# Kernel optimization log

Hardware: AMD Instinct MI355X
Metric: run time of the kernel (lower is better)

Reference implementation:

```python
import jax, jax.numpy as jnp
import numpy as np

N, IN_DIM, OUT_DIM, NUM_HOPS, SD = 8192, 256, 256, 4, 64
ETA, LAM_LAP, LAM_SP, EPS = 0.5, 0.3, 0.05, 0.5
LN_EPS = 1e-5


def setup_inputs() -> dict:
    key = jax.random.key(0)
    ks = jax.random.split(key, 6)
    K = NUM_HOPS + 1
    return {
        "H": jax.random.normal(ks[0], (N, IN_DIM), jnp.float32),
        "hops": jax.random.normal(ks[1], (K, N, IN_DIM), jnp.float32),
        "L": jax.random.normal(ks[2], (N, N), jnp.float32),
        "U": jax.random.normal(ks[3], (K, IN_DIM, SD), jnp.float32) * 0.1,
        "W_in": jax.random.normal(ks[4], (OUT_DIM, IN_DIM), jnp.float32) * 0.05,
        "ln_gamma": jnp.ones((OUT_DIM,), jnp.float32),
        "ln_beta": jnp.zeros((OUT_DIM,), jnp.float32),
        "log_tau": jnp.zeros((), jnp.float32),
    }


def _per_hop(U_k, H_k):
    n = H_k.shape[0]
    Q, _ = jnp.linalg.qr(U_k)                 # [in_dim, sd]
    Z = Q.T @ H_k.T                           # [sd, n]
    G = Z @ Z.T                               # [sd, sd] Gram, reused
    Sigma = G / (n + 1e-8)
    tr_S = jnp.trace(Sigma)
    tr_S2 = jnp.sum(Sigma * Sigma)            # trace(Sigma @ Sigma), Sigma symmetric
    rank_eff = tr_S ** 2 / (tr_S2 + 1e-8)
    coeff = SD / (n * EPS ** 2 + 1e-8)
    M = jnp.eye(SD, dtype=Z.dtype) + coeff * G
    Lc = jnp.linalg.cholesky(M)
    MiZ = jax.scipy.linalg.cho_solve((Lc, True), Z)  # [sd, n]
    grad_R = (Q @ MiZ).T                      # [n, in_dim]
    return rank_eff, grad_R


def reference(H, hops, L, U, W_in, ln_gamma, ln_beta, log_tau):
    tau = jnp.clip(jnp.exp(log_tau), 0.1, 10.0)
    rank_effs, grads_R = jax.vmap(_per_hop)(U, hops)      # [K], [K,n,in_dim]
    lap_terms = jnp.einsum('nm,kmd->knd', L, hops)        # [K,n,in_dim]
    w = jax.nn.softmax(rank_effs / tau)                   # [K]
    grad_sum = jnp.einsum('k,knd->nd', w, grads_R)
    lap_sum = jnp.einsum('k,knd->nd', w, lap_terms)
    H_half = H + ETA * grad_sum - ETA * LAM_LAP * lap_sum
    H_prox = jnp.sign(H_half) * jax.nn.relu(jnp.abs(H_half) - LAM_SP * ETA)
    H_out = H_prox @ W_in.T
    mu = jnp.mean(H_out, axis=-1, keepdims=True)
    var = jnp.var(H_out, axis=-1, keepdims=True)
    H_out = (H_out - mu) * jax.lax.rsqrt(var + LN_EPS) * ln_gamma + ln_beta
    return H_out, rank_effs, w
```

## Files before the change

kernel.cpp:

```cpp
#include <hip/hip_runtime.h>
#include <stdint.h>


typedef __attribute__((ext_vector_type(8))) short  s16x8;
typedef __attribute__((ext_vector_type(4))) float  f32x4;

#define NNODE 8192
#define DIN   256
#define KHOP  5
#define SDM   64

static const size_t OFF_Q    = 0;
static const size_t OFF_QT   = OFF_Q   + (size_t)5*256*64*4;
static const size_t OFF_ZT   = OFF_QT  + (size_t)5*64*256*2;
static const size_t OFF_GP   = OFF_ZT  + (size_t)5*8192*64*2;
static const size_t OFF_LM   = OFF_GP  + (size_t)5*16*4096*4;
static const size_t OFF_RD   = OFF_LM  + (size_t)5*4096*4;
static const size_t OFF_LU   = OFF_RD  + (size_t)5*64*4;
static const size_t OFF_RDU  = OFF_LU  + (size_t)5*4096*4;
static const size_t OFF_RE   = OFF_RDU + (size_t)5*64*4;
static const size_t OFF_W    = OFF_RE  + 64;
static const size_t OFF_T2   = OFF_W   + 64;
static const size_t OFF_HWT  = OFF_T2  + (size_t)5*256*64*2;
static const size_t OFF_WBF  = OFF_HWT + (size_t)256*8192*2;
static const size_t OFF_HP   = OFF_WBF + (size_t)256*256*2;
static const size_t OFF_PART = OFF_HP  + (size_t)8192*256*2;

__device__ __forceinline__ unsigned short f2bf(float f){
  unsigned u = __builtin_bit_cast(unsigned, f);
  u += 0x7FFFu + ((u >> 16) & 1u);
  return (unsigned short)(u >> 16);
}
__device__ __forceinline__ float bf2f(unsigned h){
  return __builtin_bit_cast(float, h << 16);
}
__device__ __forceinline__ void gl_lds16(const void* g, void* l){
  __builtin_amdgcn_global_load_lds(
      (const __attribute__((address_space(1))) void*)g,
      (__attribute__((address_space(3))) void*)l, 16, 0, 0);
}
__device__ __forceinline__ f32x4 mfma16(s16x8 a, s16x8 b, f32x4 c){
  return __builtin_amdgcn_mfma_f32_16x16x32_bf16(a, b, c, 0, 0, 0);
}
__device__ __forceinline__ int swz(int row7, int colbyte){
  return row7*128 + (colbyte ^ (row7 << 4));
}

__device__ __forceinline__ void wave_chol64(float* a, float& rdk, int lane){
  rdk = 0.0f;
  #pragma unroll
  for (int j = 0; j < 64; ++j){
    float dj  = __shfl(a[j], j);
    float d   = sqrtf(fmaxf(dj, 1e-20f));
    float rdj = 1.0f / d;
    float cj  = a[j] * rdj;
    a[j] = cj;
    if (lane == j) rdk = rdj;
    #pragma unroll
    for (int l = j+1; l < 64; ++l)
      a[l] -= cj * __shfl(cj, l);
  }
}

__global__ __launch_bounds__(256) void k_pre(const float* __restrict__ U,
                                             float* __restrict__ Lu,
                                             float* __restrict__ rdu){
  __shared__ float A[64*65];
  int tid = threadIdx.x;
  int k = blockIdx.x;
  const float* Uk = U + (size_t)k*16384;
  int ti = tid >> 4, tj = tid & 15;
  float s[16];
  #pragma unroll
  for (int i = 0; i < 16; ++i) s[i] = 0.0f;
  for (int n = 0; n < 256; ++n){
    f32x4 xa = *(const f32x4*)(Uk + n*64 + ti*4);
    f32x4 xb = *(const f32x4*)(Uk + n*64 + tj*4);
    #pragma unroll
    for (int p = 0; p < 4; ++p)
      #pragma unroll
      for (int q = 0; q < 4; ++q) s[p*4+q] += xa[p]*xb[q];
  }
  #pragma unroll
  for (int p = 0; p < 4; ++p)
    #pragma unroll
    for (int q = 0; q < 4; ++q) A[(ti*4+p)*65 + tj*4+q] = s[p*4+q];
  __syncthreads();
  if (tid < 64){
    int lane = tid;
    float a[64];
    #pragma unroll
    for (int l = 0; l < 64; ++l) a[l] = A[lane*65 + l];
    float rdk;
    wave_chol64(a, rdk, lane);
    #pragma unroll
    for (int l = 0; l < 64; ++l) Lu[(size_t)k*4096 + lane*64 + l] = a[l];
    rdu[k*64 + lane] = rdk;
  }
}

__global__ __launch_bounds__(256) void k_qsolve(const float* __restrict__ U,
                                                const float* __restrict__ Lu,
                                                const float* __restrict__ rdu,
                                                float* __restrict__ Qf,
                                                unsigned short* __restrict__ Qt){
  int k = blockIdx.y, tid = threadIdx.x, wave = tid >> 6, lane = tid & 63;
  __shared__ float Al[64*65];
  __shared__ float rds[64];
  for (int e = tid; e < 4096; e += 256) Al[(e>>6)*65 + (e&63)] = Lu[(size_t)k*4096 + e];
  if (tid < 64) rds[tid] = rdu[k*64 + tid];
  __syncthreads();
  int n = blockIdx.x*4 + wave;
  float x = U[((size_t)k*256 + n)*64 + lane];
  #pragma unroll
  for (int j = 0; j < 64; ++j){
    float zj = __shfl(x, j) * rds[j];
    x = (lane == j) ? zj : (lane > j ? x - Al[lane*65+j]*zj : x);
  }
  Qf[((size_t)k*256 + n)*64 + lane] = x;
  Qt[(size_t)k*16384 + lane*256 + n] = f2bf(x);
}

__global__ __launch_bounds__(256,2) void k_zgemm(const float* __restrict__ hops,
                                                 const unsigned short* __restrict__ Qt,
                                                 unsigned short* __restrict__ Zt){
  __shared__ __align__(16) unsigned short Al[128][72];
  __shared__ __align__(16) unsigned short Bl[64][64];
  int tid = threadIdx.x, lane = tid & 63, wave = tid >> 6;
  int q = lane >> 4, r = lane & 15;
  int k = blockIdx.y, m0 = blockIdx.x * 128;
  f32x4 acc[2][4];
  #pragma unroll
  for (int a = 0; a < 2; ++a)
    #pragma unroll
    for (int b = 0; b < 4; ++b) acc[a][b] = (f32x4){0,0,0,0};
  int rr = tid >> 1, half = tid & 1;
  for (int it = 0; it < 4; ++it){
    __syncthreads();
    #pragma unroll
    for (int i = 0; i < 2; ++i){
      int o = i*4096 + wave*1024 + lane*16;
      int srow = o >> 7, kc = (o & 127) >> 1;
      gl_lds16(Qt + (size_t)k*16384 + srow*256 + it*64 + kc,
               (char*)&Bl[0][0] + i*4096 + wave*1024);
    }
    const float* ga = hops + ((size_t)k*NNODE + m0 + rr)*256 + it*64 + half*32;
    f32x4 v[8];
    #pragma unroll
    for (int i = 0; i < 8; ++i) v[i] = *(const f32x4*)(ga + i*4);
    #pragma unroll
    for (int i = 0; i < 4; ++i){
      s16x8 t;
      #pragma unroll
      for (int j = 0; j < 8; ++j){ int e = i*8+j; t[j] = (short)f2bf(v[e>>2][e&3]); }
      *(s16x8*)&Al[rr][half*32 + i*8] = t;
    }
    __syncthreads();
    #pragma unroll
    for (int h = 0; h < 2; ++h){
      int ko = h*32 + q*8;
      s16x8 b[4];
      #pragma unroll
      for (int ni = 0; ni < 4; ++ni) b[ni] = *(const s16x8*)&Bl[ni*16 + r][ko];
      #pragma unroll
      for (int mi = 0; mi < 2; ++mi){
        s16x8 a = *(const s16x8*)&Al[wave*32 + mi*16 + r][ko];
        #pragma unroll
        for (int ni = 0; ni < 4; ++ni) acc[mi][ni] = mfma16(a, b[ni], acc[mi][ni]);
      }
    }
  }
  #pragma unroll
  for (int mi = 0; mi < 2; ++mi)
    #pragma unroll
    for (int ni = 0; ni < 4; ++ni)
      #pragma unroll
      for (int ii = 0; ii < 4; ++ii){
        int m = m0 + wave*32 + mi*16 + q*4 + ii;
        int sc = ni*16 + r;
        Zt[((size_t)k*NNODE + m)*64 + sc] = f2bf(acc[mi][ni][ii]);
      }
}

__global__ __launch_bounds__(256) void k_gpart(const unsigned short* __restrict__ Zt,
                                               float* __restrict__ Gp){
  int k = blockIdx.x, c = blockIdx.y, tid = threadIdx.x;
  __shared__ __align__(16) unsigned short Zl[128][64];
  int ti = tid >> 4, tj = tid & 15;
  float acc[16];
  #pragma unroll
  for (int i = 0; i < 16; ++i) acc[i] = 0.0f;
  for (int sub = 0; sub < 4; ++sub){
    const char* gb = (const char*)Zt + ((size_t)k*NNODE + c*512 + sub*128)*128;
    __syncthreads();
    #pragma unroll
    for (int i = 0; i < 4; ++i){
      int o = i*4096 + tid*16;
      *(uint4*)((char*)&Zl[0][0] + o) = *(const uint4*)(gb + o);
    }
    __syncthreads();
    for (int n = 0; n < 128; ++n){
      const unsigned short* row = &Zl[n][0];
      uint2 ua = *(const uint2*)(row + ti*4);
      uint2 ub = *(const uint2*)(row + tj*4);
      float xa[4] = { bf2f(ua.x & 0xffff), bf2f(ua.x >> 16), bf2f(ua.y & 0xffff), bf2f(ua.y >> 16) };
      float xb[4] = { bf2f(ub.x & 0xffff), bf2f(ub.x >> 16), bf2f(ub.y & 0xffff), bf2f(ub.y >> 16) };
      #pragma unroll
      for (int p = 0; p < 4; ++p)
        #pragma unroll
        for (int qn = 0; qn < 4; ++qn) acc[p*4+qn] += xa[p]*xb[qn];
    }
  }
  float* o = Gp + ((size_t)k*16 + c)*4096;
  #pragma unroll
  for (int p = 0; p < 4; ++p)
    #pragma unroll
    for (int qn = 0; qn < 4; ++qn) o[(ti*4+p)*64 + tj*4+qn] = acc[p*4+qn];
}

__global__ __launch_bounds__(256) void k_gred(const float* __restrict__ Gp,
                                              float* __restrict__ LmO,
                                              float* __restrict__ rdO,
                                              float* __restrict__ reO){
  int k = blockIdx.x, tid = threadIdx.x;
  __shared__ float A[64*65];
  __shared__ float red[256];
  int ti = tid >> 4, tj = tid & 15;
  float s[16];
  #pragma unroll
  for (int i = 0; i < 16; ++i) s[i] = 0.0f;
  for (int c = 0; c < 16; ++c){
    const float* g = Gp + ((size_t)k*16 + c)*4096 + (ti*4)*64 + tj*4;
    #pragma unroll
    for (int p = 0; p < 4; ++p)
      #pragma unroll
      for (int qn = 0; qn < 4; ++qn) s[p*4+qn] += g[p*64+qn];
  }
  const float sc    = 1.0f / (8192.0f + 1e-8f);
  const float coeff = 64.0f / (8192.0f*0.25f + 1e-8f);
  float trp = 0.0f, tr2p = 0.0f;
  #pragma unroll
  for (int p = 0; p < 4; ++p)
    #pragma unroll
    for (int qn = 0; qn < 4; ++qn){
      float gg = s[p*4+qn];
      float sg = gg * sc;
      tr2p += sg*sg;
      int row = ti*4+p, col = tj*4+qn;
      if (row == col) trp += sg;
      A[row*65 + col] = (row == col ? 1.0f : 0.0f) + coeff*gg;
    }
  red[tid] = trp; __syncthreads();
  for (int o = 128; o > 0; o >>= 1){ if (tid < o) red[tid] += red[tid+o]; __syncthreads(); }
  float tr = red[0]; __syncthreads();
  red[tid] = tr2p; __syncthreads();
  for (int o = 128; o > 0; o >>= 1){ if (tid < o) red[tid] += red[tid+o]; __syncthreads(); }
  float tr2 = red[0];
  if (tid == 0) reO[k] = tr*tr / (tr2 + 1e-8f);
  __syncthreads();
  if (tid < 64){
    int lane = tid;
    float a[64];
    #pragma unroll
    for (int l = 0; l < 64; ++l) a[l] = A[lane*65 + l];
    float rdk;
    wave_chol64(a, rdk, lane);
    #pragma unroll
    for (int l = 0; l < 64; ++l) LmO[(size_t)k*4096 + lane*64 + l] = a[l];
    rdO[k*64 + lane] = rdk;
  }
}

__global__ void k_soft(const float* __restrict__ re, const float* __restrict__ ltau,
                       float* __restrict__ wv, float* __restrict__ dtail){
  if (threadIdx.x == 0){
    float tau = expf(ltau[0]);
    tau = fminf(fmaxf(tau, 0.1f), 10.0f);
    float r[5], m = -1e30f;
    for (int i = 0; i < 5; ++i){ r[i] = re[i]; m = fmaxf(m, r[i]); }
    float e[5], sum = 0.0f;
    for (int i = 0; i < 5; ++i){ e[i] = expf((r[i]-m)/tau); sum += e[i]; }
    for (int i = 0; i < 5; ++i){
      float w = e[i]/sum;
      wv[i] = w; dtail[i] = r[i]; dtail[5+i] = w;
    }
  }
}

__global__ __launch_bounds__(256) void k_post(const float* __restrict__ hops,
                                              const float* __restrict__ wv,
                                              unsigned short* __restrict__ hwT,
                                              const float* __restrict__ Qf,
                                              const float* __restrict__ LmI,
                                              const float* __restrict__ rdI,
                                              unsigned short* __restrict__ T2w,
                                              const float* __restrict__ Win,
                                              unsigned short* __restrict__ Wbf){
  __shared__ float T[64*65];
  __shared__ float rds[64];
  int bid = blockIdx.x, tid = threadIdx.x;
  if (bid < 512){
    int n0 = (bid & 127)*64, d0 = (bid >> 7)*64;
    float wl[5];
    #pragma unroll
    for (int k = 0; k < 5; ++k) wl[k] = -0.15f * wv[k];
    for (int e = tid; e < 1024; e += 256){
      int row = e >> 4, c4 = (e & 15)*4;
      f32x4 acc = (f32x4){0,0,0,0};
      #pragma unroll
      for (int k = 0; k < 5; ++k){
        f32x4 v = *(const f32x4*)(hops + ((size_t)k*NNODE + n0 + row)*256 + d0 + c4);
        acc += v * wl[k];
      }
      T[row*65 + c4+0] = acc[0]; T[row*65 + c4+1] = acc[1];
      T[row*65 + c4+2] = acc[2]; T[row*65 + c4+3] = acc[3];
    }
    __syncthreads();
    for (int e = tid; e < 1024; e += 256){
      int dr = e >> 4, c4 = (e & 15)*4;
      unsigned short h0 = f2bf(T[(c4+0)*65 + dr]);
      unsigned short h1 = f2bf(T[(c4+1)*65 + dr]);
      unsigned short h2 = f2bf(T[(c4+2)*65 + dr]);
      unsigned short h3 = f2bf(T[(c4+3)*65 + dr]);
      uint2 u; u.x = (unsigned)h0 | ((unsigned)h1 << 16); u.y = (unsigned)h2 | ((unsigned)h3 << 16);
      *(uint2*)(hwT + (size_t)(d0+dr)*NNODE + n0 + c4) = u;
    }
  } else if (bid < 832){
    int i = bid - 512;
    int k = i >> 6, xb = i & 63;
    int wave = tid >> 6, lane = tid & 63;
    for (int e = tid; e < 4096; e += 256) T[(e>>6)*65 + (e&63)] = LmI[(size_t)k*4096 + e];
    if (tid < 64) rds[tid] = rdI[k*64 + tid];
    __syncthreads();
    int n = xb*4 + wave;
    float x = Qf[((size_t)k*256 + n)*64 + lane];
    #pragma unroll
    for (int j = 0; j < 64; ++j){
      float zj = __shfl(x, j) * rds[j];
      x = (lane == j) ? zj : (lane > j ? x - T[lane*65+j]*zj : x);
    }
    #pragma unroll
    for (int j = 63; j >= 0; --j){
      float yj = __shfl(x, j) * rds[j];
      x = (lane == j) ? yj : (lane < j ? x - T[j*65+lane]*yj : x);
    }
    float scale = 0.5f * wv[k];
    T2w[((size_t)k*256 + n)*64 + lane] = f2bf(scale * x);
  } else {
    int i = bid - 832;
    int e = (i*256 + tid)*4;
    f32x4 v = *(const f32x4*)(Win + e);
    uint2 u;
    u.x = (unsigned)f2bf(v[0]) | ((unsigned)f2bf(v[1]) << 16);
    u.y = (unsigned)f2bf(v[2]) | ((unsigned)f2bf(v[3]) << 16);
    *(uint2*)(Wbf + e) = u;
  }
}

__global__ __launch_bounds__(256,2) void k_grad(const unsigned short* __restrict__ Zt,
                                                const unsigned short* __restrict__ T2w,
                                                unsigned short* __restrict__ out8){
  __shared__ __align__(16) unsigned short SM[18432];
  char* Al = (char*)SM;
  char* Bl = (char*)SM + 4096;
  int tid = threadIdx.x, lane = tid & 63, wave = tid >> 6;
  int q = lane >> 4, r = lane & 15;
  int m0 = blockIdx.x * 32;
  int gr8 = lane >> 3;
  int gcS = ((lane & 7) ^ gr8) * 16;
  f32x4 acc[2][4];
  #pragma unroll
  for (int a = 0; a < 2; ++a)
    #pragma unroll
    for (int b = 0; b < 4; ++b) acc[a][b] = (f32x4){0,0,0,0};
  for (int kk = 0; kk < 5; ++kk){
    __syncthreads();
    {
      int grow = wave*8 + gr8;
      gl_lds16((const char*)Zt + ((size_t)kk*NNODE + m0 + grow)*128 + gcS,
               Al + wave*1024);
    }
    #pragma unroll
    for (int i = 0; i < 8; ++i){
      int cb = i*4 + wave;
      int grow = cb*8 + gr8;
      gl_lds16((const char*)T2w + (size_t)kk*32768 + (size_t)grow*128 + gcS,
               Bl + cb*1024);
    }
    __syncthreads();
    #pragma unroll
    for (int h = 0; h < 2; ++h){
      int kb = h*64 + q*16;
      s16x8 b[4];
      #pragma unroll
      for (int ni = 0; ni < 4; ++ni){
        int row = wave*64 + ni*16 + r;
        b[ni] = *(const s16x8*)(Bl + (row>>3)*1024 + swz(row&7, kb));
      }
      #pragma unroll
      for (int mi = 0; mi < 2; ++mi){
        int row = mi*16 + r;
        s16x8 a = *(const s16x8*)(Al + (row>>3)*1024 + swz(row&7, kb));
        #pragma unroll
        for (int ni = 0; ni < 4; ++ni) acc[mi][ni] = mfma16(a, b[ni], acc[mi][ni]);
      }
    }
  }
  #pragma unroll
  for (int mi = 0; mi < 2; ++mi)
    #pragma unroll
    for (int ni = 0; ni < 4; ++ni)
      #pragma unroll
      for (int ii = 0; ii < 4; ++ii){
        int m = m0 + mi*16 + q*4 + ii;
        int n = wave*64 + ni*16 + r;
        out8[(size_t)m*256 + n] = f2bf(acc[mi][ni][ii]);
      }
}

__global__ __launch_bounds__(512,1) void k_big(const float* __restrict__ Lf,
                                               const unsigned short* __restrict__ Bt,
                                               unsigned short* __restrict__ part){
  __shared__ __align__(16) unsigned short SM[24960];
  char* Al = (char*)SM;
  char* Bl = (char*)SM + 16*1040;
  int tid = threadIdx.x, lane = tid & 63, wave = tid >> 6;
  int q = lane >> 4, r = lane & 15;
  int wr = wave >> 2, wc = wave & 3;
  int m0 = (blockIdx.x & 63) * 128;
  int by = blockIdx.x >> 6;
  size_t kbase = (size_t)by * 1024;
  int sr = lane >> 3;
  int sc8b = ((lane & 7) ^ sr) * 8;
  int sc8a = (lane & 7) * 8;
  int adst = swz(sr, (lane & 7) * 16);
  f32x4 acc[4][4];
  #pragma unroll
  for (int a = 0; a < 4; ++a)
    #pragma unroll
    for (int b = 0; b < 4; ++b) acc[a][b] = (f32x4){0,0,0,0};
  {
    f32x4 av[2][2];
    #pragma unroll
    for (int i = 0; i < 2; ++i){
      int c = wave*2 + i;
      const float* p = Lf + (size_t)(m0 + c*8 + sr)*NNODE + kbase + sc8a;
      av[i][0] = *(const f32x4*)p;
      av[i][1] = *(const f32x4*)(p + 4);
    }
    #pragma unroll
    for (int i = 0; i < 4; ++i){
      int cb = wave*4 + i;
      gl_lds16(Bt + (size_t)(cb*8 + sr)*NNODE + kbase + sc8b,
               Bl + cb*1040);
    }
    #pragma unroll
    for (int i = 0; i < 2; ++i){
      int c = wave*2 + i;
      s16x8 t;
      #pragma unroll
      for (int e = 0; e < 8; ++e) t[e] = (short)f2bf(av[i][e>>2][e&3]);
      *(s16x8*)(Al + c*1040 + adst) = t;
    }
    __syncthreads();
  }
  for (int t = 0; t < 16; ++t){
    size_t kn = kbase + (size_t)(t+1)*64;
    f32x4 av[2][2];
    if (t < 15){
      #pragma unroll
      for (int i = 0; i < 2; ++i){
        int c = wave*2 + i;
        const float* p = Lf + (size_t)(m0 + c*8 + sr)*NNODE + kn + sc8a;
        av[i][0] = *(const f32x4*)p;
        av[i][1] = *(const f32x4*)(p + 4);
      }
    }
    #pragma unroll
    for (int h = 0; h < 2; ++h){
      int kb = h*64 + q*16;
      s16x8 b[4];
      #pragma unroll
      for (int ni = 0; ni < 4; ++ni){
        int d = wc*64 + ni*16 + r;
        b[ni] = *(const s16x8*)(Bl + (d>>3)*1040 + swz(d&7, kb));
      }
      #pragma unroll
      for (int mi = 0; mi < 4; ++mi){
        int m = wr*64 + mi*16 + r;
        s16x8 a = *(const s16x8*)(Al + (m>>3)*1040 + swz(m&7, kb));
        #pragma unroll
        for (int ni = 0; ni < 4; ++ni) acc[mi][ni] = mfma16(a, b[ni], acc[mi][ni]);
      }
    }
    __syncthreads();
    if (t < 15){
      #pragma unroll
      for (int i = 0; i < 4; ++i){
        int cb = wave*4 + i;
        gl_lds16(Bt + (size_t)(cb*8 + sr)*NNODE + kn + sc8b,
                 Bl + cb*1040);
      }
      #pragma unroll
      for (int i = 0; i < 2; ++i){
        int c = wave*2 + i;
        s16x8 tt;
        #pragma unroll
        for (int e = 0; e < 8; ++e) tt[e] = (short)f2bf(av[i][e>>2][e&3]);
        *(s16x8*)(Al + c*1040 + adst) = tt;
      }
    }
    __syncthreads();
  }
  unsigned short* o = part + (size_t)by * 2097152;
  #pragma unroll
  for (int mi = 0; mi < 4; ++mi)
    #pragma unroll
    for (int ni = 0; ni < 4; ++ni)
      #pragma unroll
      for (int ii = 0; ii < 4; ++ii){
        int m = m0 + wr*64 + mi*16 + q*4 + ii;
        int n = wc*64 + ni*16 + r;
        o[(size_t)m*256 + n] = f2bf(acc[mi][ni][ii]);
      }
}

__global__ __launch_bounds__(256,2) void k_finln(const float* __restrict__ H,
                                                 const unsigned short* __restrict__ part,
                                                 const unsigned short* __restrict__ Wbf,
                                                 const float* __restrict__ gamma,
                                                 const float* __restrict__ beta,
                                                 float* __restrict__ out){
  __shared__ __align__(16) unsigned short Hl[64][264];
  __shared__ __align__(16) unsigned short Bl[256][64];
  __shared__ float SmR[64][4];
  __shared__ float SqR[64][4];
  int tid = threadIdx.x, lane = tid & 63, wave = tid >> 6;
  int q = lane >> 4, r = lane & 15;
  int m0 = blockIdx.x * 64;
  #define PROX(a) ({ float _t = fabsf(a) - 0.025f; _t > 0.0f ? copysignf(_t,(a)) : 0.0f; })
  for (int g = tid; g < 4096; g += 256){
    int row = g >> 6, c4 = (g & 63) * 4;
    size_t e = (size_t)(m0 + row)*256 + c4;
    f32x4 h = *(const f32x4*)(H + e);
    float s0 = h[0], s1 = h[1], s2 = h[2], s3 = h[3];
    #pragma unroll
    for (int sl = 0; sl < 9; ++sl){
      uint2 u = *(const uint2*)(part + (size_t)sl*2097152 + e);
      s0 += bf2f(u.x & 0xffff); s1 += bf2f(u.x >> 16);
      s2 += bf2f(u.y & 0xffff); s3 += bf2f(u.y >> 16);
    }
    uint2 o;
    o.x = (unsigned)f2bf(PROX(s0)) | ((unsigned)f2bf(PROX(s1)) << 16);
    o.y = (unsigned)f2bf(PROX(s2)) | ((unsigned)f2bf(PROX(s3)) << 16);
    *(uint2*)&Hl[row][c4] = o;
  }
  f32x4 acc[4][4];
  #pragma unroll
  for (int a = 0; a < 4; ++a)
    #pragma unroll
    for (int b = 0; b < 4; ++b) acc[a][b] = (f32x4){0,0,0,0};
  for (int it = 0; it < 4; ++it){
    __syncthreads();
    #pragma unroll
    for (int i = 0; i < 8; ++i){
      int o = i*4096 + wave*1024 + lane*16;
      int n = o >> 7, kc = o & 127;
      gl_lds16((const char*)Wbf + (size_t)n*512 + it*128 + kc,
               (char*)&Bl[0][0] + i*4096 + wave*1024);
    }
    __syncthreads();
    #pragma unroll
    for (int h = 0; h < 2; ++h){
      int ko = it*64 + h*32 + q*8;
      s16x8 b[4];
      #pragma unroll
      for (int ni = 0; ni < 4; ++ni) b[ni] = *(const s16x8*)&Bl[wave*64 + ni*16 + r][h*32 + q*8];
      #pragma unroll
      for (int mi = 0; mi < 4; ++mi){
        s16x8 a = *(const s16x8*)&Hl[mi*16 + r][ko];
        #pragma unroll
        for (int ni = 0; ni < 4; ++ni) acc[mi][ni] = mfma16(a, b[ni], acc[mi][ni]);
      }
    }
  }
  #pragma unroll
  for (int mi = 0; mi < 4; ++mi)
    #pragma unroll
    for (int ii = 0; ii < 4; ++ii){
      float sm = 0.0f, sq = 0.0f;
      #pragma unroll
      for (int ni = 0; ni < 4; ++ni){
        float v = acc[mi][ni][ii];
        sm += v; sq += v*v;
      }
      #pragma unroll
      for (int o = 1; o < 16; o <<= 1){ sm += __shfl_xor(sm, o, 64); sq += __shfl_xor(sq, o, 64); }
      if (r == 0){
        int rl = mi*16 + q*4 + ii;
        SmR[rl][wave] = sm; SqR[rl][wave] = sq;
      }
    }
  __syncthreads();
  float g[4], b[4];
  #pragma unroll
  for (int ni = 0; ni < 4; ++ni){
    g[ni] = gamma[wave*64 + ni*16 + r];
    b[ni] = beta [wave*64 + ni*16 + r];
  }
  #pragma unroll
  for (int mi = 0; mi < 4; ++mi)
    #pragma unroll
    for (int ii = 0; ii < 4; ++ii){
      int rl = mi*16 + q*4 + ii;
      float sm = SmR[rl][0] + SmR[rl][1] + SmR[rl][2] + SmR[rl][3];
      float sq = SqR[rl][0] + SqR[rl][1] + SqR[rl][2] + SqR[rl][3];
      float mean = sm * (1.0f/256.0f);
      float var  = sq * (1.0f/256.0f) - mean*mean;
      float rs   = rsqrtf(var + 1e-5f);
      #pragma unroll
      for (int ni = 0; ni < 4; ++ni){
        out[(size_t)(m0+rl)*256 + wave*64 + ni*16 + r] =
            (acc[mi][ni][ii] - mean)*rs*g[ni] + b[ni];
      }
    }
}

extern "C" void kernel_launch(void* const* d_in, const int* in_sizes, int n_in,
                              void* d_out, int out_size, void* d_ws, size_t ws_size,
                              hipStream_t stream){
  const float* H    = (const float*)d_in[0];
  const float* hops = (const float*)d_in[1];
  const float* Lmat = (const float*)d_in[2];
  const float* U    = (const float*)d_in[3];
  const float* Win  = (const float*)d_in[4];
  const float* gam  = (const float*)d_in[5];
  const float* bet  = (const float*)d_in[6];
  const float* ltau = (const float*)d_in[7];
  float* out = (float*)d_out;

  char* ws = (char*)d_ws;
  float*          Qf   = (float*)(ws + OFF_Q);
  unsigned short* Qt   = (unsigned short*)(ws + OFF_QT);
  unsigned short* Zt   = (unsigned short*)(ws + OFF_ZT);
  float*          Gp   = (float*)(ws + OFF_GP);
  float*          Lm   = (float*)(ws + OFF_LM);
  float*          rdw  = (float*)(ws + OFF_RD);
  float*          Lu   = (float*)(ws + OFF_LU);
  float*          rdu  = (float*)(ws + OFF_RDU);
  float*          re   = (float*)(ws + OFF_RE);
  float*          wv   = (float*)(ws + OFF_W);
  unsigned short* T2w  = (unsigned short*)(ws + OFF_T2);
  unsigned short* hwT  = (unsigned short*)(ws + OFF_HWT);
  unsigned short* Wbf  = (unsigned short*)(ws + OFF_WBF);
  unsigned short* part = (unsigned short*)(ws + OFF_PART);

  hipLaunchKernelGGL(k_pre,    dim3(5),      dim3(256), 0, stream, U, Lu, rdu);
  hipLaunchKernelGGL(k_qsolve, dim3(64,5),   dim3(256), 0, stream, U, Lu, rdu, Qf, Qt);
  hipLaunchKernelGGL(k_zgemm,  dim3(64,5),   dim3(256), 0, stream, hops, Qt, Zt);
  hipLaunchKernelGGL(k_gpart,  dim3(5,16),   dim3(256), 0, stream, Zt, Gp);
  hipLaunchKernelGGL(k_gred,   dim3(5),      dim3(256), 0, stream, Gp, Lm, rdw, re);
  hipLaunchKernelGGL(k_soft,   dim3(1),      dim3(64),  0, stream, re, ltau, wv, out + 2097152);
  hipLaunchKernelGGL(k_post,   dim3(896),    dim3(256), 0, stream, hops, wv, hwT, Qf, Lm, rdw, T2w, Win, Wbf);
  hipLaunchKernelGGL(k_grad,   dim3(256),    dim3(256), 0, stream, Zt, T2w, part + (size_t)8*2097152);
  hipLaunchKernelGGL(k_big,    dim3(512),    dim3(512), 0, stream, Lmat, hwT, part);
  hipLaunchKernelGGL(k_finln,  dim3(128),    dim3(256), 0, stream, H, part, Wbf, gam, bet, out);
}
```

Before: 649.2 us.

## Fuse Gram partials into Z GEMM and triple-buffer the big Laplacian GEMM

The Gram partial computation now runs inside k_zgemm on the bf16 Z tile it already holds in shared memory, which removes the separate k_gpart launch and its re-read of Zt. The cost is 64 partials per hop instead of 16, so k_gred has more to reduce. k_big moves from a single LDS buffer with two barriers per step to a three-stage ring, prefetching two k-steps ahead with explicit vmcnt/lgkmcnt waits and one barrier per step. Launch bounds rise to 2 blocks per CU, although the larger shared-memory footprint (about 150 KB) may not allow that occupancy.

```diff
diff --git a/kernel.cpp b/kernel.cpp
--- a/kernel.cpp
+++ b/kernel.cpp
@@ -14,7 +14,7 @@
 static const size_t OFF_QT   = OFF_Q   + (size_t)5*256*64*4;
 static const size_t OFF_ZT   = OFF_QT  + (size_t)5*64*256*2;
 static const size_t OFF_GP   = OFF_ZT  + (size_t)5*8192*64*2;
-static const size_t OFF_LM   = OFF_GP  + (size_t)5*16*4096*4;
+static const size_t OFF_LM   = OFF_GP  + (size_t)5*64*4096*4;
 static const size_t OFF_RD   = OFF_LM  + (size_t)5*4096*4;
 static const size_t OFF_LU   = OFF_RD  + (size_t)5*64*4;
 static const size_t OFF_RDU  = OFF_LU  + (size_t)5*4096*4;
@@ -123,7 +123,8 @@
 
 __global__ __launch_bounds__(256,2) void k_zgemm(const float* __restrict__ hops,
                                                  const unsigned short* __restrict__ Qt,
-                                                 unsigned short* __restrict__ Zt){
+                                                 unsigned short* __restrict__ Zt,
+                                                 float* __restrict__ Gp){
   __shared__ __align__(16) unsigned short Al[128][72];
   __shared__ __align__(16) unsigned short Bl[64][64];
   int tid = threadIdx.x, lane = tid & 63, wave = tid >> 6;
@@ -176,46 +177,33 @@
     for (int ni = 0; ni < 4; ++ni)
       #pragma unroll
       for (int ii = 0; ii < 4; ++ii){
-        int m = m0 + wave*32 + mi*16 + q*4 + ii;
+        int ml = wave*32 + mi*16 + q*4 + ii;
         int sc = ni*16 + r;
-        Zt[((size_t)k*NNODE + m)*64 + sc] = f2bf(acc[mi][ni][ii]);
-      }
-}
-
-__global__ __launch_bounds__(256) void k_gpart(const unsigned short* __restrict__ Zt,
-                                               float* __restrict__ Gp){
-  int k = blockIdx.x, c = blockIdx.y, tid = threadIdx.x;
-  __shared__ __align__(16) unsigned short Zl[128][64];
+        unsigned short v = f2bf(acc[mi][ni][ii]);
+        Zt[((size_t)k*NNODE + m0 + ml)*64 + sc] = v;
+        Al[ml][sc] = v;
+      }
+  __syncthreads();
   int ti = tid >> 4, tj = tid & 15;
-  float acc[16];
-  #pragma unroll
-  for (int i = 0; i < 16; ++i) acc[i] = 0.0f;
-  for (int sub = 0; sub < 4; ++sub){
-    const char* gb = (const char*)Zt + ((size_t)k*NNODE + c*512 + sub*128)*128;
-    __syncthreads();
-    #pragma unroll
-    for (int i = 0; i < 4; ++i){
-      int o = i*4096 + tid*16;
-      *(uint4*)((char*)&Zl[0][0] + o) = *(const uint4*)(gb + o);
-    }
-    __syncthreads();
-    for (int n = 0; n < 128; ++n){
-      const unsigned short* row = &Zl[n][0];
-      uint2 ua = *(const uint2*)(row + ti*4);
-      uint2 ub = *(const uint2*)(row + tj*4);
-      float xa[4] = { bf2f(ua.x & 0xffff), bf2f(ua.x >> 16), bf2f(ua.y & 0xffff), bf2f(ua.y >> 16) };
-      float xb[4] = { bf2f(ub.x & 0xffff), bf2f(ub.x >> 16), bf2f(ub.y & 0xffff), bf2f(ub.y >> 16) };
-      #pragma unroll
-      for (int p = 0; p < 4; ++p)
-        #pragma unroll
-        for (int qn = 0; qn < 4; ++qn) acc[p*4+qn] += xa[p]*xb[qn];
-    }
-  }
-  float* o = Gp + ((size_t)k*16 + c)*4096;
+  float g16[16];
+  #pragma unroll
+  for (int i = 0; i < 16; ++i) g16[i] = 0.0f;
+  for (int n = 0; n < 128; ++n){
+    const unsigned short* row = &Al[n][0];
+    uint2 ua = *(const uint2*)(row + ti*4);
+    uint2 ub = *(const uint2*)(row + tj*4);
+    float xa[4] = { bf2f(ua.x & 0xffff), bf2f(ua.x >> 16), bf2f(ua.y & 0xffff), bf2f(ua.y >> 16) };
+    float xb[4] = { bf2f(ub.x & 0xffff), bf2f(ub.x >> 16), bf2f(ub.y & 0xffff), bf2f(ub.y >> 16) };
+    #pragma unroll
+    for (int p = 0; p < 4; ++p)
+      #pragma unroll
+      for (int qn = 0; qn < 4; ++qn) g16[p*4+qn] += xa[p]*xb[qn];
+  }
+  float* go = Gp + ((size_t)(k*64 + blockIdx.x))*4096;
   #pragma unroll
   for (int p = 0; p < 4; ++p)
     #pragma unroll
-    for (int qn = 0; qn < 4; ++qn) o[(ti*4+p)*64 + tj*4+qn] = acc[p*4+qn];
+    for (int qn = 0; qn < 4; ++qn) go[(ti*4+p)*64 + tj*4+qn] = g16[p*4+qn];
 }
 
 __global__ __launch_bounds__(256) void k_gred(const float* __restrict__ Gp,
@@ -229,8 +217,8 @@
   float s[16];
   #pragma unroll
   for (int i = 0; i < 16; ++i) s[i] = 0.0f;
-  for (int c = 0; c < 16; ++c){
-    const float* g = Gp + ((size_t)k*16 + c)*4096 + (ti*4)*64 + tj*4;
+  for (int c = 0; c < 64; ++c){
+    const float* g = Gp + ((size_t)(k*64 + c))*4096 + (ti*4)*64 + tj*4;
     #pragma unroll
     for (int p = 0; p < 4; ++p)
       #pragma unroll
@@ -418,12 +406,13 @@
       }
 }
 
-__global__ __launch_bounds__(512,1) void k_big(const float* __restrict__ Lf,
+__global__ __launch_bounds__(512,2) void k_big(const float* __restrict__ Lf,
                                                const unsigned short* __restrict__ Bt,
                                                unsigned short* __restrict__ part){
-  __shared__ __align__(16) unsigned short SM[24960];
-  char* Al = (char*)SM;
-  char* Bl = (char*)SM + 16*1040;
+  __shared__ __align__(16) unsigned short SM[74880];
+  char* SMb = (char*)SM;
+  const int CH48 = 48*1040;
+  const int BOFF = 16*1040;
   int tid = threadIdx.x, lane = tid & 63, wave = tid >> 6;
   int q = lane >> 4, r = lane & 15;
   int wr = wave >> 2, wc = wave & 3;
@@ -431,7 +420,7 @@
   int by = blockIdx.x >> 6;
   size_t kbase = (size_t)by * 1024;
   int sr = lane >> 3;
-  int sc8b = ((lane & 7) ^ sr) * 8;
+  int scS  = ((lane & 7) ^ sr) * 8;
   int sc8a = (lane & 7) * 8;
   int adst = swz(sr, (lane & 7) * 16);
   f32x4 acc[4][4];
@@ -439,41 +428,76 @@
   for (int a = 0; a < 4; ++a)
     #pragma unroll
     for (int b = 0; b < 4; ++b) acc[a][b] = (f32x4){0,0,0,0};
+  f32x4 av[2][2];
   {
-    f32x4 av[2][2];
+    f32x4 av0[2][2];
     #pragma unroll
     for (int i = 0; i < 2; ++i){
       int c = wave*2 + i;
       const float* p = Lf + (size_t)(m0 + c*8 + sr)*NNODE + kbase + sc8a;
+      av0[i][0] = *(const f32x4*)p;
+      av0[i][1] = *(const f32x4*)(p + 4);
+    }
+    #pragma unroll
+    for (int i = 0; i < 4; ++i){
+      int cb = wave*4 + i;
+      gl_lds16(Bt + (size_t)(cb*8 + sr)*NNODE + kbase + scS,
+               SMb + 0*CH48 + BOFF + cb*1040);
+    }
+    #pragma unroll
+    for (int i = 0; i < 2; ++i){
+      int c = wave*2 + i;
+      const float* p = Lf + (size_t)(m0 + c*8 + sr)*NNODE + (kbase + 64) + sc8a;
       av[i][0] = *(const f32x4*)p;
       av[i][1] = *(const f32x4*)(p + 4);
     }
     #pragma unroll
     for (int i = 0; i < 4; ++i){
       int cb = wave*4 + i;
-      gl_lds16(Bt + (size_t)(cb*8 + sr)*NNODE + kbase + sc8b,
-               Bl + cb*1040);
-    }
+      gl_lds16(Bt + (size_t)(cb*8 + sr)*NNODE + (kbase + 64) + scS,
+               SMb + 1*CH48 + BOFF + cb*1040);
+    }
+    asm volatile("s_waitcnt vmcnt(12)" ::: "memory");
+    __builtin_amdgcn_sched_barrier(0);
     #pragma unroll
     for (int i = 0; i < 2; ++i){
       int c = wave*2 + i;
       s16x8 t;
       #pragma unroll
+      for (int e = 0; e < 8; ++e) t[e] = (short)f2bf(av0[i][e>>2][e&3]);
+      *(s16x8*)(SMb + 0*CH48 + c*1040 + adst) = t;
+    }
+    asm volatile("s_waitcnt vmcnt(4)" ::: "memory");
+    __builtin_amdgcn_sched_barrier(0);
+    #pragma unroll
+    for (int i = 0; i < 2; ++i){
+      int c = wave*2 + i;
+      s16x8 t;
+      #pragma unroll
       for (int e = 0; e < 8; ++e) t[e] = (short)f2bf(av[i][e>>2][e&3]);
-      *(s16x8*)(Al + c*1040 + adst) = t;
-    }
-    __syncthreads();
+      *(s16x8*)(SMb + 1*CH48 + c*1040 + adst) = t;
+    }
+    asm volatile("s_waitcnt lgkmcnt(0)" ::: "memory");
+    __builtin_amdgcn_sched_barrier(0);
+    __builtin_amdgcn_s_barrier();
   }
   for (int t = 0; t < 16; ++t){
-    size_t kn = kbase + (size_t)(t+1)*64;
-    f32x4 av[2][2];
-    if (t < 15){
+    char* cbuf = SMb + (t % 3)*CH48;
+    char* nbuf = SMb + ((t + 2) % 3)*CH48;
+    if (t < 14){
+      size_t k2 = kbase + (size_t)(t+2)*64;
       #pragma unroll
       for (int i = 0; i < 2; ++i){
         int c = wave*2 + i;
-        const float* p = Lf + (size_t)(m0 + c*8 + sr)*NNODE + kn + sc8a;
+        const float* p = Lf + (size_t)(m0 + c*8 + sr)*NNODE + k2 + sc8a;
         av[i][0] = *(const f32x4*)p;
         av[i][1] = *(const f32x4*)(p + 4);
+      }
+      #pragma unroll
+      for (int i = 0; i < 4; ++i){
+        int cb = wave*4 + i;
+        gl_lds16(Bt + (size_t)(cb*8 + sr)*NNODE + k2 + scS,
+                 nbuf + BOFF + cb*1040);
       }
     }
     #pragma unroll
@@ -483,34 +507,34 @@
       #pragma unroll
       for (int ni = 0; ni < 4; ++ni){
         int d = wc*64 + ni*16 + r;
-        b[ni] = *(const s16x8*)(Bl + (d>>3)*1040 + swz(d&7, kb));
+        b[ni] = *(const s16x8*)(cbuf + BOFF + (d>>3)*1040 + swz(d&7, kb));
       }
       #pragma unroll
       for (int mi = 0; mi < 4; ++mi){
         int m = wr*64 + mi*16 + r;
-        s16x8 a = *(const s16x8*)(Al + (m>>3)*1040 + swz(m&7, kb));
+        s16x8 a = *(const s16x8*)(cbuf + (m>>3)*1040 + swz(m&7, kb));
         #pragma unroll
         for (int ni = 0; ni < 4; ++ni) acc[mi][ni] = mfma16(a, b[ni], acc[mi][ni]);
       }
     }
-    __syncthreads();
-    if (t < 15){
-      #pragma unroll
-      for (int i = 0; i < 4; ++i){
-        int cb = wave*4 + i;
-        gl_lds16(Bt + (size_t)(cb*8 + sr)*NNODE + kn + sc8b,
-                 Bl + cb*1040);
-      }
+    if (t < 14){
+      asm volatile("s_waitcnt vmcnt(4)" ::: "memory");
+      __builtin_amdgcn_sched_barrier(0);
       #pragma unroll
       for (int i = 0; i < 2; ++i){
         int c = wave*2 + i;
         s16x8 tt;
         #pragma unroll
         for (int e = 0; e < 8; ++e) tt[e] = (short)f2bf(av[i][e>>2][e&3]);
-        *(s16x8*)(Al + c*1040 + adst) = tt;
-      }
-    }
-    __syncthreads();
+        *(s16x8*)(nbuf + c*1040 + adst) = tt;
+      }
+      asm volatile("s_waitcnt lgkmcnt(0)" ::: "memory");
+      __builtin_amdgcn_sched_barrier(0);
+    } else if (t == 14){
+      asm volatile("s_waitcnt vmcnt(0) lgkmcnt(0)" ::: "memory");
+      __builtin_amdgcn_sched_barrier(0);
+    }
+    if (t < 15) __builtin_amdgcn_s_barrier();
   }
   unsigned short* o = part + (size_t)by * 2097152;
   #pragma unroll
@@ -657,8 +681,7 @@
 
   hipLaunchKernelGGL(k_pre,    dim3(5),      dim3(256), 0, stream, U, Lu, rdu);
   hipLaunchKernelGGL(k_qsolve, dim3(64,5),   dim3(256), 0, stream, U, Lu, rdu, Qf, Qt);
-  hipLaunchKernelGGL(k_zgemm,  dim3(64,5),   dim3(256), 0, stream, hops, Qt, Zt);
-  hipLaunchKernelGGL(k_gpart,  dim3(5,16),   dim3(256), 0, stream, Zt, Gp);
+  hipLaunchKernelGGL(k_zgemm,  dim3(64,5),   dim3(256), 0, stream, hops, Qt, Zt, Gp);
   hipLaunchKernelGGL(k_gred,   dim3(5),      dim3(256), 0, stream, Gp, Lm, rdw, re);
   hipLaunchKernelGGL(k_soft,   dim3(1),      dim3(64),  0, stream, re, ltau, wv, out + 2097152);
   hipLaunchKernelGGL(k_post,   dim3(896),    dim3(256), 0, stream, hops, wv, hwT, Qf, Lm, rdw, T2w, Win, Wbf);
```

Result: no change. 649.9 us (+0.1%).

## Fuse Gram partials into Z GEMM and retile big L GEMM

Applied to the files above, without the earlier changes.

The Gram partial computation moves into the Z GEMM epilogue. Each block writes its Z tile to LDS and computes a 64x64 partial Gram from it, which removes the separate k_gpart kernel and its re-read of Zt. k_gred now reduces 64 partials instead of 16. The large L x hops GEMM is retiled from 512-thread blocks with 128x256 tiles and K-step 64 to 256-thread blocks with 64x256 tiles, K-step 32 and a new swizzle, using less LDS so more blocks fit per CU. The smaller tiles reduce reuse of each loaded tile and add more barrier iterations.

```diff
diff --git a/kernel.cpp b/kernel.cpp
--- a/kernel.cpp
+++ b/kernel.cpp
@@ -14,7 +14,7 @@
 static const size_t OFF_QT   = OFF_Q   + (size_t)5*256*64*4;
 static const size_t OFF_ZT   = OFF_QT  + (size_t)5*64*256*2;
 static const size_t OFF_GP   = OFF_ZT  + (size_t)5*8192*64*2;
-static const size_t OFF_LM   = OFF_GP  + (size_t)5*16*4096*4;
+static const size_t OFF_LM   = OFF_GP  + (size_t)5*64*4096*4;
 static const size_t OFF_RD   = OFF_LM  + (size_t)5*4096*4;
 static const size_t OFF_LU   = OFF_RD  + (size_t)5*64*4;
 static const size_t OFF_RDU  = OFF_LU  + (size_t)5*4096*4;
@@ -44,6 +44,10 @@
 }
 __device__ __forceinline__ int swz(int row7, int colbyte){
   return row7*128 + (colbyte ^ (row7 << 4));
+}
+__device__ __forceinline__ int swz32(int row16, int colbyte){
+  int g = ((colbyte >> 4) ^ row16) & 3;
+  return row16*64 + (g << 4) + (colbyte & 15);
 }
 
 __device__ __forceinline__ void wave_chol64(float* a, float& rdk, int lane){
@@ -123,7 +127,8 @@
 
 __global__ __launch_bounds__(256,2) void k_zgemm(const float* __restrict__ hops,
                                                  const unsigned short* __restrict__ Qt,
-                                                 unsigned short* __restrict__ Zt){
+                                                 unsigned short* __restrict__ Zt,
+                                                 float* __restrict__ Gp){
   __shared__ __align__(16) unsigned short Al[128][72];
   __shared__ __align__(16) unsigned short Bl[64][64];
   int tid = threadIdx.x, lane = tid & 63, wave = tid >> 6;
@@ -176,46 +181,33 @@
     for (int ni = 0; ni < 4; ++ni)
       #pragma unroll
       for (int ii = 0; ii < 4; ++ii){
-        int m = m0 + wave*32 + mi*16 + q*4 + ii;
+        int ml = wave*32 + mi*16 + q*4 + ii;
         int sc = ni*16 + r;
-        Zt[((size_t)k*NNODE + m)*64 + sc] = f2bf(acc[mi][ni][ii]);
-      }
-}
-
-__global__ __launch_bounds__(256) void k_gpart(const unsigned short* __restrict__ Zt,
-                                               float* __restrict__ Gp){
-  int k = blockIdx.x, c = blockIdx.y, tid = threadIdx.x;
-  __shared__ __align__(16) unsigned short Zl[128][64];
+        unsigned short v = f2bf(acc[mi][ni][ii]);
+        Zt[((size_t)k*NNODE + m0 + ml)*64 + sc] = v;
+        Al[ml][sc] = v;
+      }
+  __syncthreads();
   int ti = tid >> 4, tj = tid & 15;
-  float acc[16];
-  #pragma unroll
-  for (int i = 0; i < 16; ++i) acc[i] = 0.0f;
-  for (int sub = 0; sub < 4; ++sub){
-    const char* gb = (const char*)Zt + ((size_t)k*NNODE + c*512 + sub*128)*128;
-    __syncthreads();
-    #pragma unroll
-    for (int i = 0; i < 4; ++i){
-      int o = i*4096 + tid*16;
-      *(uint4*)((char*)&Zl[0][0] + o) = *(const uint4*)(gb + o);
-    }
-    __syncthreads();
-    for (int n = 0; n < 128; ++n){
-      const unsigned short* row = &Zl[n][0];
-      uint2 ua = *(const uint2*)(row + ti*4);
-      uint2 ub = *(const uint2*)(row + tj*4);
-      float xa[4] = { bf2f(ua.x & 0xffff), bf2f(ua.x >> 16), bf2f(ua.y & 0xffff), bf2f(ua.y >> 16) };
-      float xb[4] = { bf2f(ub.x & 0xffff), bf2f(ub.x >> 16), bf2f(ub.y & 0xffff), bf2f(ub.y >> 16) };
-      #pragma unroll
-      for (int p = 0; p < 4; ++p)
-        #pragma unroll
-        for (int qn = 0; qn < 4; ++qn) acc[p*4+qn] += xa[p]*xb[qn];
-    }
-  }
-  float* o = Gp + ((size_t)k*16 + c)*4096;
+  float g16[16];
+  #pragma unroll
+  for (int i = 0; i < 16; ++i) g16[i] = 0.0f;
+  for (int n = 0; n < 128; ++n){
+    const unsigned short* row = &Al[n][0];
+    uint2 ua = *(const uint2*)(row + ti*4);
+    uint2 ub = *(const uint2*)(row + tj*4);
+    float xa[4] = { bf2f(ua.x & 0xffff), bf2f(ua.x >> 16), bf2f(ua.y & 0xffff), bf2f(ua.y >> 16) };
+    float xb[4] = { bf2f(ub.x & 0xffff), bf2f(ub.x >> 16), bf2f(ub.y & 0xffff), bf2f(ub.y >> 16) };
+    #pragma unroll
+    for (int p = 0; p < 4; ++p)
+      #pragma unroll
+      for (int qn = 0; qn < 4; ++qn) g16[p*4+qn] += xa[p]*xb[qn];
+  }
+  float* go = Gp + ((size_t)(k*64 + blockIdx.x))*4096;
   #pragma unroll
   for (int p = 0; p < 4; ++p)
     #pragma unroll
-    for (int qn = 0; qn < 4; ++qn) o[(ti*4+p)*64 + tj*4+qn] = acc[p*4+qn];
+    for (int qn = 0; qn < 4; ++qn) go[(ti*4+p)*64 + tj*4+qn] = g16[p*4+qn];
 }
 
 __global__ __launch_bounds__(256) void k_gred(const float* __restrict__ Gp,
@@ -229,8 +221,8 @@
   float s[16];
   #pragma unroll
   for (int i = 0; i < 16; ++i) s[i] = 0.0f;
-  for (int c = 0; c < 16; ++c){
-    const float* g = Gp + ((size_t)k*16 + c)*4096 + (ti*4)*64 + tj*4;
+  for (int c = 0; c < 64; ++c){
+    const float* g = Gp + ((size_t)(k*64 + c))*4096 + (ti*4)*64 + tj*4;
     #pragma unroll
     for (int p = 0; p < 4; ++p)
       #pragma unroll
@@ -418,97 +410,74 @@
       }
 }
 
-__global__ __launch_bounds__(512,1) void k_big(const float* __restrict__ Lf,
+__global__ __launch_bounds__(256,4) void k_big(const float* __restrict__ Lf,
                                                const unsigned short* __restrict__ Bt,
                                                unsigned short* __restrict__ part){
-  __shared__ __align__(16) unsigned short SM[24960];
+  __shared__ __align__(16) unsigned short SM[10240];
   char* Al = (char*)SM;
-  char* Bl = (char*)SM + 16*1040;
+  char* Bl = (char*)SM + 4096;
   int tid = threadIdx.x, lane = tid & 63, wave = tid >> 6;
   int q = lane >> 4, r = lane & 15;
-  int wr = wave >> 2, wc = wave & 3;
-  int m0 = (blockIdx.x & 63) * 128;
-  int by = blockIdx.x >> 6;
+  int m0 = (blockIdx.x & 127) * 64;
+  int by = blockIdx.x >> 7;
   size_t kbase = (size_t)by * 1024;
-  int sr = lane >> 3;
-  int sc8b = ((lane & 7) ^ sr) * 8;
-  int sc8a = (lane & 7) * 8;
-  int adst = swz(sr, (lane & 7) * 16);
+  int ar = tid >> 2, aq = tid & 3;
+  int adst = (ar >> 4)*1024 + (ar & 15)*64 + (((aq ^ (ar & 3)) & 3) << 4);
+  const float* abase = Lf + (size_t)(m0 + ar)*NNODE + aq*8;
+  int br16 = lane >> 2;
+  int bsrcS = (((lane & 3) ^ (br16 & 3)) & 3) * 8;
   f32x4 acc[4][4];
   #pragma unroll
   for (int a = 0; a < 4; ++a)
     #pragma unroll
     for (int b = 0; b < 4; ++b) acc[a][b] = (f32x4){0,0,0,0};
   {
-    f32x4 av[2][2];
-    #pragma unroll
-    for (int i = 0; i < 2; ++i){
-      int c = wave*2 + i;
-      const float* p = Lf + (size_t)(m0 + c*8 + sr)*NNODE + kbase + sc8a;
-      av[i][0] = *(const f32x4*)p;
-      av[i][1] = *(const f32x4*)(p + 4);
-    }
+    f32x4 v0 = *(const f32x4*)(abase + kbase);
+    f32x4 v1 = *(const f32x4*)(abase + kbase + 4);
     #pragma unroll
     for (int i = 0; i < 4; ++i){
-      int cb = wave*4 + i;
-      gl_lds16(Bt + (size_t)(cb*8 + sr)*NNODE + kbase + sc8b,
-               Bl + cb*1040);
-    }
-    #pragma unroll
-    for (int i = 0; i < 2; ++i){
-      int c = wave*2 + i;
-      s16x8 t;
-      #pragma unroll
-      for (int e = 0; e < 8; ++e) t[e] = (short)f2bf(av[i][e>>2][e&3]);
-      *(s16x8*)(Al + c*1040 + adst) = t;
-    }
-    __syncthreads();
-  }
-  for (int t = 0; t < 16; ++t){
-    size_t kn = kbase + (size_t)(t+1)*64;
-    f32x4 av[2][2];
-    if (t < 15){
-      #pragma unroll
-      for (int i = 0; i < 2; ++i){
-        int c = wave*2 + i;
-        const float* p = Lf + (size_t)(m0 + c*8 + sr)*NNODE + kn + sc8a;
-        av[i][0] = *(const f32x4*)p;
-        av[i][1] = *(const f32x4*)(p + 4);
-      }
-    }
-    #pragma unroll
-    for (int h = 0; h < 2; ++h){
-      int kb = h*64 + q*16;
-      s16x8 b[4];
-      #pragma unroll
-      for (int ni = 0; ni < 4; ++ni){
-        int d = wc*64 + ni*16 + r;
-        b[ni] = *(const s16x8*)(Bl + (d>>3)*1040 + swz(d&7, kb));
-      }
-      #pragma unroll
-      for (int mi = 0; mi < 4; ++mi){
-        int m = wr*64 + mi*16 + r;
-        s16x8 a = *(const s16x8*)(Al + (m>>3)*1040 + swz(m&7, kb));
-        #pragma unroll
-        for (int ni = 0; ni < 4; ++ni) acc[mi][ni] = mfma16(a, b[ni], acc[mi][ni]);
-      }
-    }
-    __syncthreads();
-    if (t < 15){
+      int cb = i*4 + wave;
+      gl_lds16(Bt + (size_t)(cb*16 + br16)*NNODE + kbase + bsrcS,
+               Bl + cb*1024 + lane*16);
+    }
+    s16x8 t;
+    #pragma unroll
+    for (int e = 0; e < 8; ++e) t[e] = (short)f2bf((e < 4 ? v0 : v1)[e & 3]);
+    *(s16x8*)(Al + adst) = t;
+    __syncthreads();
+  }
+  for (int t = 0; t < 32; ++t){
+    size_t kn = kbase + (size_t)(t+1)*32;
+    f32x4 v0, v1;
+    if (t < 31){
+      v0 = *(const f32x4*)(abase + kn);
+      v1 = *(const f32x4*)(abase + kn + 4);
+    }
+    int gbyte = (((q ^ (r & 3)) & 3) << 4);
+    s16x8 b[4];
+    #pragma unroll
+    for (int ni = 0; ni < 4; ++ni){
+      int d = wave*64 + ni*16 + r;
+      b[ni] = *(const s16x8*)(Bl + (d >> 4)*1024 + (d & 15)*64 + gbyte);
+    }
+    #pragma unroll
+    for (int mi = 0; mi < 4; ++mi){
+      s16x8 a = *(const s16x8*)(Al + mi*1024 + r*64 + gbyte);
+      #pragma unroll
+      for (int ni = 0; ni < 4; ++ni) acc[mi][ni] = mfma16(a, b[ni], acc[mi][ni]);
+    }
+    __syncthreads();
+    if (t < 31){
       #pragma unroll
       for (int i = 0; i < 4; ++i){
-        int cb = wave*4 + i;
-        gl_lds16(Bt + (size_t)(cb*8 + sr)*NNODE + kn + sc8b,
-                 Bl + cb*1040);
-      }
-      #pragma unroll
-      for (int i = 0; i < 2; ++i){
-        int c = wave*2 + i;
-        s16x8 tt;
-        #pragma unroll
-        for (int e = 0; e < 8; ++e) tt[e] = (short)f2bf(av[i][e>>2][e&3]);
-        *(s16x8*)(Al + c*1040 + adst) = tt;
-      }
+        int cb = i*4 + wave;
+        gl_lds16(Bt + (size_t)(cb*16 + br16)*NNODE + kn + bsrcS,
+                 Bl + cb*1024 + lane*16);
+      }
+      s16x8 tt;
+      #pragma unroll
+      for (int e = 0; e < 8; ++e) tt[e] = (short)f2bf((e < 4 ? v0 : v1)[e & 3]);
+      *(s16x8*)(Al + adst) = tt;
     }
     __syncthreads();
   }
@@ -519,8 +488,8 @@
     for (int ni = 0; ni < 4; ++ni)
       #pragma unroll
       for (int ii = 0; ii < 4; ++ii){
-        int m = m0 + wr*64 + mi*16 + q*4 + ii;
-        int n = wc*64 + ni*16 + r;
+        int m = m0 + mi*16 + q*4 + ii;
+        int n = wave*64 + ni*16 + r;
         o[(size_t)m*256 + n] = f2bf(acc[mi][ni][ii]);
       }
 }
@@ -657,12 +626,11 @@
 
   hipLaunchKernelGGL(k_pre,    dim3(5),      dim3(256), 0, stream, U, Lu, rdu);
   hipLaunchKernelGGL(k_qsolve, dim3(64,5),   dim3(256), 0, stream, U, Lu, rdu, Qf, Qt);
-  hipLaunchKernelGGL(k_zgemm,  dim3(64,5),   dim3(256), 0, stream, hops, Qt, Zt);
-  hipLaunchKernelGGL(k_gpart,  dim3(5,16),   dim3(256), 0, stream, Zt, Gp);
+  hipLaunchKernelGGL(k_zgemm,  dim3(64,5),   dim3(256), 0, stream, hops, Qt, Zt, Gp);
   hipLaunchKernelGGL(k_gred,   dim3(5),      dim3(256), 0, stream, Gp, Lm, rdw, re);
   hipLaunchKernelGGL(k_soft,   dim3(1),      dim3(64),  0, stream, re, ltau, wv, out + 2097152);
   hipLaunchKernelGGL(k_post,   dim3(896),    dim3(256), 0, stream, hops, wv, hwT, Qf, Lm, rdw, T2w, Win, Wbf);
   hipLaunchKernelGGL(k_grad,   dim3(256),    dim3(256), 0, stream, Zt, T2w, part + (size_t)8*2097152);
-  hipLaunchKernelGGL(k_big,    dim3(512),    dim3(512), 0, stream, Lmat, hwT, part);
+  hipLaunchKernelGGL(k_big,    dim3(1024),   dim3(256), 0, stream, Lmat, hwT, part);
   hipLaunchKernelGGL(k_finln,  dim3(128),    dim3(256), 0, stream, H, part, Wbf, gam, bet, out);
 }
```

New measurement: 872.4 us. 1.34x slower.
